# Kernel optimization log

Hardware: AMD Instinct MI355X
Metric: run time of the kernel (lower is better)

## Reference

```python
import jax, jax.numpy as jnp
import numpy as np

D_MODEL = 1024
NUM_HEADS = 16
D_K = D_MODEL // NUM_HEADS
B, S = 2, 2048


def setup_inputs() -> dict:
    key = jax.random.key(0)
    ks = jax.random.split(key, 13)
    s = 1.0 / np.sqrt(D_MODEL)
    inp = {
        "query": jax.random.normal(ks[0], (B, S, D_MODEL), jnp.float32),
        "key_": jax.random.normal(ks[1], (B, S, D_MODEL), jnp.float32),
        "value": jax.random.normal(ks[2], (B, S, D_MODEL), jnp.float32),
        "mask": jax.random.randint(ks[3], (B, 1, 1, S), 0, 2, jnp.int32),
        # torch nn.Linear convention: weight (out, in), y = x @ W.T + b
        "Wq": jax.random.uniform(ks[4], (D_MODEL, D_MODEL), jnp.float32, -s, s),
        "bq": jax.random.uniform(ks[5], (D_MODEL,), jnp.float32, -s, s),
        "Wk": jax.random.uniform(ks[6], (D_MODEL, D_MODEL), jnp.float32, -s, s),
        "bk": jax.random.uniform(ks[7], (D_MODEL,), jnp.float32, -s, s),
        "Wv": jax.random.uniform(ks[8], (D_MODEL, D_MODEL), jnp.float32, -s, s),
        "bv": jax.random.uniform(ks[9], (D_MODEL,), jnp.float32, -s, s),
        "Wo": jax.random.uniform(ks[10], (D_MODEL, D_MODEL), jnp.float32, -s, s),
        "bo": jax.random.uniform(ks[11], (D_MODEL,), jnp.float32, -s, s),
    }
    return inp


def _split_heads(x):
    b, s, _ = x.shape
    return x.reshape(b, s, NUM_HEADS, D_K).transpose(0, 2, 1, 3)  # (B,H,S,dk)


def reference(query, key_, value, mask, Wq, bq, Wk, bk, Wv, bv, Wo, bo):
    Q = _split_heads(query @ Wq.T + bq)
    K = _split_heads(key_ @ Wk.T + bk)
    V = _split_heads(value @ Wv.T + bv)
    scores = jnp.einsum("bhqd,bhkd->bhqk", Q, K) / np.sqrt(D_K).astype(np.float32)
    scores = jnp.where(mask == 0, -jnp.inf, scores)
    attn = jax.nn.softmax(scores, axis=-1)
    attn = jnp.nan_to_num(attn)  # fully-masked rows -> 0 (matches torch.nan_to_num)
    ctx = jnp.einsum("bhqk,bhkd->bhqd", attn, V)
    concat = ctx.transpose(0, 2, 1, 3).reshape(query.shape[0], -1, D_MODEL)
    out = concat @ Wo.T + bo  # dropout is identity in eval mode
    return out
```

## Files before the change

### kernel.cpp

```cpp
#include <hip/hip_runtime.h>
#include <math.h>

#define D_MODEL 1024
#define NUM_HEADS 16
#define DK 64
#define BATCH 2
#define SEQ 2048

using f32x4  = __attribute__((ext_vector_type(4))) float;
using f16x8  = __attribute__((ext_vector_type(8))) _Float16;

__device__ __forceinline__ void gl_lds16(const void* g, void* l) {
    __builtin_amdgcn_global_load_lds(
        (const __attribute__((address_space(1))) void*)g,
        (__attribute__((address_space(3))) void*)l, 16, 0, 0);
}

__global__ __launch_bounds__(256) void mask_scan_kernel(
    const int* __restrict__ mask, int* __restrict__ pos, int* __restrict__ nc)
{
    const int b = blockIdx.x;
    const int tid = threadIdx.x;
    __shared__ int sums[256];
    int v[8]; int cnt = 0;
    const int base = b * SEQ + tid * 8;
    #pragma unroll
    for (int e = 0; e < 8; ++e) { v[e] = (mask[base + e] != 0) ? 1 : 0; cnt += v[e]; }
    sums[tid] = cnt;
    __syncthreads();
    for (int off = 1; off < 256; off <<= 1) {
        int t = (tid >= off) ? sums[tid - off] : 0;
        __syncthreads();
        sums[tid] += t;
        __syncthreads();
    }
    int run = sums[tid] - cnt;
    #pragma unroll
    for (int e = 0; e < 8; ++e) { pos[base + e] = run; run += v[e]; }
    if (tid == 255) nc[b] = sums[255];
}

template <int COMPACT>
__global__ __launch_bounds__(256) void conv_f16_kernel(
    const float* s0, const float* s1, const float* s2, const float* s3,
    _Float16* d0, _Float16* d1, _Float16* d2, _Float16* d3,
    int rows, const int* __restrict__ mask, const int* __restrict__ pos)
{
    const int y = blockIdx.y;
    const float* src = (y == 0) ? s0 : (y == 1) ? s1 : (y == 2) ? s2 : s3;
    _Float16* dst = (y == 0) ? d0 : (y == 1) ? d1 : (y == 2) ? d2 : d3;
    const int id = blockIdx.x * 256 + threadIdx.x;
    if (id >= rows * 128) return;
    const int row = id >> 7;
    int drow = row;
    if (COMPACT && y != 0) {
        if (!mask[row]) return;
        drow = (row >> 11) * SEQ + pos[row];
    }
    const int s  = id & 127;
    const int g  = s >> 3, ss = s & 7;
    const int lb = ss ^ (drow & 7);

    const float* p = src + (size_t)row * 1024 + g * 64 + lb * 8;
    const float4 a = *(const float4*)p;
    const float4 bq = *(const float4*)(p + 4);
    f16x8 o;
    o[0] = (_Float16)a.x;  o[1] = (_Float16)a.y;
    o[2] = (_Float16)a.z;  o[3] = (_Float16)a.w;
    o[4] = (_Float16)bq.x; o[5] = (_Float16)bq.y;
    o[6] = (_Float16)bq.z; o[7] = (_Float16)bq.w;
    *(f16x8*)&dst[(size_t)drow * 1024 + s * 8] = o;
}

template <int MODE>
__global__ __launch_bounds__(256) void mfma_gemm_f16_kernel(
    const _Float16* __restrict__ A2, const _Float16* __restrict__ W2,
    const float* __restrict__ bias, float* __restrict__ Cf,
    _Float16* __restrict__ Ch, const int* __restrict__ ncArr)
{
    constexpr int KS = 1024;
    __shared__ f16x8 Asl[3][1024];
    __shared__ f16x8 Bsl[3][512];

    const int bm = blockIdx.x * 128, bn = blockIdx.y * 64;
    if (MODE == 2 || MODE == 3) {
        if ((bm & (SEQ - 1)) >= ncArr[bm >> 11]) return;
    }

    const int tid = threadIdx.x;
    const int wv = tid >> 6, ln = tid & 63;
    const int wm = wv >> 1, wn = wv & 1;
    const int x = ln & 15, y = ln >> 4;

    f32x4 acc[4][2] = {};

    const _Float16* Ab = A2 + (size_t)bm * KS;
    const _Float16* Bb = W2 + (size_t)bn * KS;
    const int srow = ln >> 3;
    const int scol = (ln & 7) * 8;

    auto stage = [&](int bufi, int kt) {
        #pragma unroll
        for (int c = 0; c < 4; ++c) {
            const int rowb = wv * 32 + c * 8;
            gl_lds16(Ab + (size_t)(rowb + srow) * KS + kt * 64 + scol,
                     &Asl[bufi][rowb << 3]);
        }
        #pragma unroll
        for (int c = 0; c < 2; ++c) {
            const int rowb = wv * 16 + c * 8;
            gl_lds16(Bb + (size_t)(rowb + srow) * KS + kt * 64 + scol,
                     &Bsl[bufi][rowb << 3]);
        }
    };

    stage(0, 0);
    stage(1, 1);

    int buf = 0, sbuf = 2;
    for (int kt = 0; kt < 16; ++kt) {
        if (kt < 15) asm volatile("s_waitcnt vmcnt(6)" ::: "memory");
        else         asm volatile("s_waitcnt vmcnt(0)" ::: "memory");
        __builtin_amdgcn_s_barrier();
        if (kt + 2 < 16) stage(sbuf, kt + 2);
        #pragma unroll
        for (int half = 0; half < 2; ++half) {
            f16x8 af[4], bfr[2];
            #pragma unroll
            for (int mf = 0; mf < 4; ++mf) {
                const int r = wm * 64 + mf * 16 + x;
                af[mf] = Asl[buf][(r << 3) | ((half * 4 + y) ^ (r & 7))];
            }
            #pragma unroll
            for (int nf = 0; nf < 2; ++nf) {
                const int r = wn * 32 + nf * 16 + x;
                bfr[nf] = Bsl[buf][(r << 3) | ((half * 4 + y) ^ (r & 7))];
            }
            #pragma unroll
            for (int mf = 0; mf < 4; ++mf)
                #pragma unroll
                for (int nf = 0; nf < 2; ++nf)
                    acc[mf][nf] = __builtin_amdgcn_mfma_f32_16x16x32_f16(
                        af[mf], bfr[nf], acc[mf][nf], 0, 0, 0);
        }
        buf  = (buf  == 2) ? 0 : buf  + 1;
        sbuf = (sbuf == 2) ? 0 : sbuf + 1;
    }

    #pragma unroll
    for (int nf = 0; nf < 2; ++nf) {
        const int n = bn + wn * 32 + nf * 16 + x;
        const float bv = bias[n];
        #pragma unroll
        for (int mf = 0; mf < 4; ++mf) {
            const int mbase = bm + wm * 64 + mf * 16 + y * 4;
            #pragma unroll
            for (int r = 0; r < 4; ++r) {
                const int m = mbase + r;
                const float v = acc[mf][nf][r] + bv;
                const int b = m >> 11, s = m & (SEQ - 1);
                const int hh = n >> 6, dd = n & 63;
                if (MODE == 0) {
                    Cf[(size_t)m * D_MODEL + n] = v;
                } else if (MODE == 1) {
                    const int blk = (dd >> 3) ^ (s & 7), i = dd & 7;
                    Ch[((size_t)((b * NUM_HEADS + hh) * SEQ + s)) * 64 +
                       blk * 8 + i] = (_Float16)(v * 0.125f);
                } else if (MODE == 2) {
                    if (s < ncArr[b]) {
                        const int blk = (dd >> 3) ^ (s & 7), i = dd & 7;
                        Ch[((size_t)((b * NUM_HEADS + hh) * SEQ + s)) * 64 +
                           blk * 8 + i] = (_Float16)v;
                    }
                } else {
                    if (s < ncArr[b]) {
                        const int tile = s >> 6, w = s & 63;
                        const int blk = (w >> 3) ^ (dd & 7), i = w & 7;
                        Ch[((size_t)((b * NUM_HEADS + hh) * DK + dd)) * SEQ +
                           tile * 64 + blk * 8 + i] = (_Float16)v;
                    }
                }
            }
        }
    }
}

__global__ __launch_bounds__(256, 3) void attn_mfma_kernel(
    const _Float16* __restrict__ Q2, const _Float16* __restrict__ K2,
    const _Float16* __restrict__ VT2, const int* __restrict__ ncArr,
    _Float16* __restrict__ ACT)
{
    __shared__ __align__(16) _Float16 SM[20480];

    const int tid = threadIdx.x;
    const int wave = tid >> 6, lane = tid & 63;
    const int lo4 = lane & 15, hi4 = lane >> 4;
    _Float16* Pw = SM + 16384 + wave * 1024;

    const int orig = blockIdx.x;
    const int swz = (orig & 7) * 128 + (orig >> 3);
    const int bh = swz >> 5, qblk = swz & 31;
    const int b = bh >> 4, h = bh & 15;

    const _Float16* Kb = K2 + (size_t)bh * SEQ * 64;
    const _Float16* Vb = VT2 + (size_t)bh * DK * SEQ;

    const int ncb = ncArr[b];
    const int ntiles = (ncb + 63) >> 6;

    const int qr = qblk * 64 + wave * 16 + lo4;
    const _Float16* Q2row = Q2 + (size_t)(bh * SEQ + qr) * 64;
    f16x8 qf[2];
    #pragma unroll
    for (int c = 0; c < 2; ++c)
        qf[c] = *(const f16x8*)&Q2row[(((c * 4 + hi4) ^ (qr & 7)) * 8)];

    auto stage_kv = [&](int base, int k0) {
        #pragma unroll
        for (int j = 0; j < 4; ++j) {
            const int g = j * 256 + wave * 64;
            const int gi = g + lane;
            const _Float16* src;
            if (gi < 512) {
                src = Kb + (size_t)(k0 + (gi >> 3)) * 64 + (gi & 7) * 8;
            } else {
                const int g2 = gi - 512;
                src = Vb + (size_t)(g2 >> 3) * SEQ + k0 + (g2 & 7) * 8;
            }
            gl_lds16(src, SM + base + (size_t)g * 8);
        }
    };

    f32x4 ctx[4] = {};
    float m = -INFINITY, l = 0.f;

    stage_kv(0, 0);
    for (int t = 0; t < ntiles; ++t) {
        if (t + 1 < ntiles) {
            stage_kv(((t + 1) & 1) * 8192, (t + 1) * 64);
            asm volatile("s_waitcnt vmcnt(4)" ::: "memory");
        } else {
            asm volatile("s_waitcnt vmcnt(0)" ::: "memory");
        }
        __builtin_amdgcn_s_barrier();

        const _Float16* Ks = SM + (t & 1) * 8192;
        const _Float16* VTs = Ks + 4096;
        const int k0 = t * 64;

        f32x4 sc[4];
        __builtin_amdgcn_s_setprio(1);
        #pragma unroll
        for (int kt = 0; kt < 4; ++kt) {
            f32x4 s = {0.f, 0.f, 0.f, 0.f};
            const int row = kt * 16 + lo4;
            const int rx = row & 7;
            #pragma unroll
            for (int c = 0; c < 2; ++c) {
                const f16x8 kf = *(f16x8*)&Ks[row * 64 + (((c * 4 + hi4) ^ rx) * 8)];
                s = __builtin_amdgcn_mfma_f32_16x16x32_f16(kf, qf[c], s, 0, 0, 0);
            }
            sc[kt] = s;
        }
        __builtin_amdgcn_s_setprio(0);

        float cmax = -1e30f;
        if (k0 + 64 <= ncb) {
            #pragma unroll
            for (int kt = 0; kt < 4; ++kt)
                #pragma unroll
                for (int r = 0; r < 4; ++r) cmax = fmaxf(cmax, sc[kt][r]);
        } else {
            #pragma unroll
            for (int kt = 0; kt < 4; ++kt)
                #pragma unroll
                for (int r = 0; r < 4; ++r) {
                    const int kidx = k0 + kt * 16 + hi4 * 4 + r;
                    const float sv = (kidx < ncb) ? sc[kt][r] : -1e30f;
                    sc[kt][r] = sv;
                    cmax = fmaxf(cmax, sv);
                }
        }
        cmax = fmaxf(cmax, __shfl_xor(cmax, 16));
        cmax = fmaxf(cmax, __shfl_xor(cmax, 32));

        const float mnew = fmaxf(m, cmax);
        const float e1 = __expf(m - mnew);
        m = mnew;

        float ps = 0.f;
        #pragma unroll
        for (int kt = 0; kt < 4; ++kt) {
            const float pv0 = __expf(sc[kt][0] - mnew);
            const float pv1 = __expf(sc[kt][1] - mnew);
            const float pv2 = __expf(sc[kt][2] - mnew);
            const float pv3 = __expf(sc[kt][3] - mnew);
            ps += (pv0 + pv1) + (pv2 + pv3);
            union { _Float16 hh[2]; unsigned u; } pk0, pk1;
            pk0.hh[0] = (_Float16)pv0; pk0.hh[1] = (_Float16)pv1;
            pk1.hh[0] = (_Float16)pv2; pk1.hh[1] = (_Float16)pv3;
            const int blk16 = (kt * 2 + (hi4 >> 1)) ^ (lo4 & 7);
            unsigned* dst = (unsigned*)&Pw[lo4 * 64 + blk16 * 8 + (hi4 & 1) * 4];
            dst[0] = pk0.u; dst[1] = pk1.u;
        }
        ps += __shfl_xor(ps, 16);
        ps += __shfl_xor(ps, 32);
        l = l * e1 + ps;

        #pragma unroll
        for (int dt = 0; dt < 4; ++dt)
            #pragma unroll
            for (int r = 0; r < 4; ++r) ctx[dt][r] *= e1;

        __builtin_amdgcn_s_setprio(1);
        #pragma unroll
        for (int c = 0; c < 2; ++c) {
            const f16x8 pf = *(f16x8*)&Pw[lo4 * 64 + (((c * 4 + hi4) ^ (lo4 & 7)) * 8)];
            #pragma unroll
            for (int dt = 0; dt < 4; ++dt) {
                const int row = dt * 16 + lo4;
                const f16x8 vf =
                    *(f16x8*)&VTs[row * 64 + (((c * 4 + hi4) ^ (row & 7)) * 8)];
                ctx[dt] = __builtin_amdgcn_mfma_f32_16x16x32_f16(vf, pf, ctx[dt], 0, 0, 0);
            }
        }
        __builtin_amdgcn_s_setprio(0);

        __builtin_amdgcn_s_barrier();
    }

    __syncthreads();
    const float inv = (l > 0.f) ? (1.f / l) : 0.f;
    float* OutL = (float*)SM;
    #pragma unroll
    for (int dt = 0; dt < 4; ++dt)
        #pragma unroll
        for (int r = 0; r < 4; ++r)
            OutL[(wave * 16 + lo4) * 68 + dt * 16 + hi4 * 4 + r] = ctx[dt][r] * inv;
    __syncthreads();
    {
        const int row = tid >> 2, cb = (tid & 3) * 16;
        const int mrow = b * SEQ + qblk * 64 + row;
        _Float16* arow = ACT + (size_t)mrow * 1024;
        #pragma unroll
        for (int u = 0; u < 2; ++u) {
            const int lb = (cb >> 3) + u;
            const int ss = lb ^ (mrow & 7);
            f16x8 hv;
            #pragma unroll
            for (int i = 0; i < 8; ++i)
                hv[i] = (_Float16)OutL[row * 68 + cb + u * 8 + i];
            *(f16x8*)&arow[h * 64 + ss * 8] = hv;
        }
    }
}

template <int SPLIT>
__global__ __launch_bounds__(256) void gemm_bias_kernel(
    const float* __restrict__ A, const float* __restrict__ W,
    const float* __restrict__ bias, float* __restrict__ C,
    int M, int N, int K)
{
    constexpr int TILE = 64, KT = 16;
    __shared__ float As[KT][TILE + 4];
    __shared__ float Ws[KT][TILE + 4];
    const int tid = threadIdx.x;
    const int tx = tid & 15, ty = tid >> 4;
    const int bm = blockIdx.x * TILE, bn = blockIdx.y * TILE;
    const int lrow = tid >> 2, lk4 = (tid & 3) << 2;
    float acc[4][4] = {{0.f}};
    for (int k0 = 0; k0 < K; k0 += KT) {
        const float4 a4 = *(const float4*)&A[(size_t)(bm + lrow) * K + k0 + lk4];
        const float4 w4 = *(const float4*)&W[(size_t)(bn + lrow) * K + k0 + lk4];
        __syncthreads();
        As[lk4 + 0][lrow] = a4.x; As[lk4 + 1][lrow] = a4.y;
        As[lk4 + 2][lrow] = a4.z; As[lk4 + 3][lrow] = a4.w;
        Ws[lk4 + 0][lrow] = w4.x; Ws[lk4 + 1][lrow] = w4.y;
        Ws[lk4 + 2][lrow] = w4.z; Ws[lk4 + 3][lrow] = w4.w;
        __syncthreads();
        #pragma unroll
        for (int kk = 0; kk < KT; ++kk) {
            const float4 av = *(const float4*)&As[kk][ty << 2];
            const float4 wv = *(const float4*)&Ws[kk][tx << 2];
            acc[0][0] += av.x * wv.x; acc[0][1] += av.x * wv.y; acc[0][2] += av.x * wv.z; acc[0][3] += av.x * wv.w;
            acc[1][0] += av.y * wv.x; acc[1][1] += av.y * wv.y; acc[1][2] += av.y * wv.z; acc[1][3] += av.y * wv.w;
            acc[2][0] += av.z * wv.x; acc[2][1] += av.z * wv.y; acc[2][2] += av.z * wv.z; acc[2][3] += av.z * wv.w;
            acc[3][0] += av.w * wv.x; acc[3][1] += av.w * wv.y; acc[3][2] += av.w * wv.z; acc[3][3] += av.w * wv.w;
        }
    }
    const float4 bb = *(const float4*)&bias[bn + (tx << 2)];
    #pragma unroll
    for (int i = 0; i < 4; ++i) {
        const int row = bm + (ty << 2) + i;
        float4 o;
        o.x = acc[i][0] + bb.x; o.y = acc[i][1] + bb.y;
        o.z = acc[i][2] + bb.z; o.w = acc[i][3] + bb.w;
        if (SPLIT) {
            const int b = row >> 11, s = row & (SEQ - 1), hh = bn >> 6;
            *(float4*)&C[((size_t)((b * NUM_HEADS + hh) * SEQ + s)) * DK + (tx << 2)] = o;
        } else {
            *(float4*)&C[(size_t)row * N + bn + (tx << 2)] = o;
        }
    }
}

__global__ __launch_bounds__(256, 2) void attn_fp32_kernel(
    const float* __restrict__ Q, const float* __restrict__ K,
    const float* __restrict__ V, const int* __restrict__ mask,
    float* __restrict__ OUT)
{
    const int qb = blockIdx.x, h = blockIdx.y, b = blockIdx.z;
    const int wave = threadIdx.x >> 6, lane = threadIdx.x & 63;
    const int tid = threadIdx.x;
    const int bh = b * NUM_HEADS + h;
    const float* Qb = Q + (size_t)bh * SEQ * DK;
    const float* Kb = K + (size_t)bh * SEQ * DK;
    const float* Vb = V + (size_t)bh * SEQ * DK;
    const int* mb = mask + b * SEQ;
    __shared__ float Ks[64][68];
    __shared__ float Vs[64][68];
    const int row = qb * 256 + wave * 64 + lane;
    float q[DK], ctx[DK];
    #pragma unroll
    for (int d4 = 0; d4 < 16; ++d4) {
        const float4 t = *(const float4*)&Qb[(size_t)row * DK + 4 * d4];
        q[4*d4] = t.x; q[4*d4+1] = t.y; q[4*d4+2] = t.z; q[4*d4+3] = t.w;
        ctx[4*d4] = 0.f; ctx[4*d4+1] = 0.f; ctx[4*d4+2] = 0.f; ctx[4*d4+3] = 0.f;
    }
    float m = -INFINITY, l = 0.f;
    for (int t = 0; t < SEQ / 64; ++t) {
        const int k0 = t * 64;
        const float* Kt = Kb + (size_t)k0 * DK;
        const float* Vt = Vb + (size_t)k0 * DK;
        __syncthreads();
        #pragma unroll
        for (int i = 0; i < 4; ++i) {
            const int f4 = i * 256 + tid;
            const int r = f4 >> 4, c = (f4 & 15) << 2;
            *(float4*)&Ks[r][c] = *(const float4*)&Kt[4 * f4];
            *(float4*)&Vs[r][c] = *(const float4*)&Vt[4 * f4];
        }
        __syncthreads();
        const unsigned long long mbits = __ballot(mb[k0 + lane] != 0);
        if (mbits == 0ULL) continue;
        for (int c0 = 0; c0 < 64; c0 += 16) {
            const unsigned bits = (unsigned)((mbits >> c0) & 0xFFFFULL);
            if (!bits) continue;
            float sc[16];
            #pragma unroll
            for (int j = 0; j < 16; ++j) {
                if (!((bits >> j) & 1u)) { sc[j] = -INFINITY; continue; }
                float a0 = 0.f, a1 = 0.f, a2 = 0.f, a3 = 0.f;
                #pragma unroll
                for (int d4 = 0; d4 < 16; ++d4) {
                    const float4 kv = *(const float4*)&Ks[c0 + j][4 * d4];
                    a0 += q[4*d4] * kv.x; a1 += q[4*d4+1] * kv.y;
                    a2 += q[4*d4+2] * kv.z; a3 += q[4*d4+3] * kv.w;
                }
                sc[j] = ((a0 + a1) + (a2 + a3)) * 0.125f;
            }
            float cmax = sc[0];
            #pragma unroll
            for (int j = 1; j < 16; ++j) cmax = fmaxf(cmax, sc[j]);
            if (cmax > m) {
                const float scale = __expf(m - cmax);
                l *= scale;
                #pragma unroll
                for (int d = 0; d < DK; ++d) ctx[d] *= scale;
                m = cmax;
            }
            #pragma unroll
            for (int j = 0; j < 16; ++j) {
                if (!((bits >> j) & 1u)) continue;
                const float p = __expf(sc[j] - m);
                l += p;
                #pragma unroll
                for (int d4 = 0; d4 < 16; ++d4) {
                    const float4 vv = *(const float4*)&Vs[c0 + j][4 * d4];
                    ctx[4*d4] += p * vv.x; ctx[4*d4+1] += p * vv.y;
                    ctx[4*d4+2] += p * vv.z; ctx[4*d4+3] += p * vv.w;
                }
            }
        }
    }
    const float inv = (l > 0.f) ? (1.f / l) : 0.f;
    float* dst = OUT + ((size_t)(b * SEQ + row)) * D_MODEL + h * DK;
    #pragma unroll
    for (int d4 = 0; d4 < 16; ++d4) {
        float4 o;
        o.x = ctx[4*d4] * inv; o.y = ctx[4*d4+1] * inv;
        o.z = ctx[4*d4+2] * inv; o.w = ctx[4*d4+3] * inv;
        *(float4*)&dst[4 * d4] = o;
    }
}

extern "C" void kernel_launch(void* const* d_in, const int* in_sizes, int n_in,
                              void* d_out, int out_size, void* d_ws, size_t ws_size,
                              hipStream_t stream)
{
    const float* query = (const float*)d_in[0];
    const float* key_  = (const float*)d_in[1];
    const float* value = (const float*)d_in[2];
    const int*   mask  = (const int*)d_in[3];
    const float* Wq = (const float*)d_in[4];
    const float* bq = (const float*)d_in[5];
    const float* Wk = (const float*)d_in[6];
    const float* bk = (const float*)d_in[7];
    const float* Wv = (const float*)d_in[8];
    const float* bv = (const float*)d_in[9];
    const float* Wo = (const float*)d_in[10];
    const float* bo = (const float*)d_in[11];
    float* out = (float*)d_out;

    const int M = BATCH * SEQ;
    const size_t ACT_B = (size_t)M * 1024 * 2;
    const size_t W_B   = (size_t)D_MODEL * 1024 * 2;
    const size_t K2_B  = (size_t)32 * SEQ * 64 * 2;
    const size_t VT2_B = (size_t)32 * DK * SEQ * 2;
    const size_t Q2_B  = K2_B;
    const size_t POS_B = (size_t)BATCH * SEQ * 4 + 256;

    char* base = (char*)d_ws;
    _Float16* actQh = (_Float16*)(base);
    _Float16* actKh = (_Float16*)(base + ACT_B);
    _Float16* actVh = (_Float16*)(base + 2 * ACT_B);
    _Float16* actO  = (_Float16*)(base + 3 * ACT_B);
    _Float16* w2qh  = (_Float16*)(base + 4 * ACT_B);
    _Float16* w2kh  = (_Float16*)((char*)w2qh + W_B);
    _Float16* w2vh  = (_Float16*)((char*)w2kh + W_B);
    _Float16* w2oh  = (_Float16*)((char*)w2vh + W_B);
    _Float16* k2    = (_Float16*)((char*)w2oh + W_B);
    _Float16* vt2   = (_Float16*)((char*)k2 + K2_B);
    _Float16* q2    = (_Float16*)((char*)vt2 + VT2_B);
    int* posArr = (int*)((char*)q2 + Q2_B);
    int* ncArr  = posArr + BATCH * SEQ;
    const size_t need = 4 * ACT_B + 4 * W_B + K2_B + VT2_B + Q2_B + POS_B;

    if (ws_size >= need) {
        mask_scan_kernel<<<BATCH, 256, 0, stream>>>(mask, posArr, ncArr);

        conv_f16_kernel<0><<<dim3(D_MODEL / 2, 4), 256, 0, stream>>>(
            Wq, Wk, Wv, Wo, w2qh, w2kh, w2vh, w2oh, D_MODEL, nullptr, nullptr);

        conv_f16_kernel<1><<<dim3(M / 2, 3), 256, 0, stream>>>(
            query, key_, value, nullptr, actQh, actKh, actVh, nullptr,
            M, mask, posArr);

        dim3 ggrid(M / 128, D_MODEL / 64);
        mfma_gemm_f16_kernel<2><<<ggrid, 256, 0, stream>>>(
            actKh, w2kh, bk, nullptr, k2, ncArr);
        mfma_gemm_f16_kernel<3><<<ggrid, 256, 0, stream>>>(
            actVh, w2vh, bv, nullptr, vt2, ncArr);
        mfma_gemm_f16_kernel<1><<<ggrid, 256, 0, stream>>>(
            actQh, w2qh, bq, nullptr, q2, ncArr);

        attn_mfma_kernel<<<1024, 256, 0, stream>>>(q2, k2, vt2, ncArr, actO);

        mfma_gemm_f16_kernel<0><<<ggrid, 256, 0, stream>>>(
            actO, w2oh, bo, out, nullptr, ncArr);
    } else {
        float* q_ws = (float*)(base);
        float* k_ws = (float*)(base + (size_t)M * D_MODEL * 4);
        float* v_ws = (float*)(base + 2 * (size_t)M * D_MODEL * 4);
        float* c_ws = (float*)(base + 3 * (size_t)M * D_MODEL * 4);
        dim3 ggrid(M / 64, D_MODEL / 64);
        gemm_bias_kernel<1><<<ggrid, 256, 0, stream>>>(query, Wq, bq, q_ws, M, D_MODEL, D_MODEL);
        gemm_bias_kernel<1><<<ggrid, 256, 0, stream>>>(key_,  Wk, bk, k_ws, M, D_MODEL, D_MODEL);
        gemm_bias_kernel<1><<<ggrid, 256, 0, stream>>>(value, Wv, bv, v_ws, M, D_MODEL, D_MODEL);
        dim3 agrid(SEQ / 256, NUM_HEADS, BATCH);
        attn_fp32_kernel<<<agrid, 256, 0, stream>>>(q_ws, k_ws, v_ws, mask, c_ws);
        gemm_bias_kernel<0><<<ggrid, 256, 0, stream>>>(c_ws, Wo, bo, out, M, D_MODEL, D_MODEL);
    }
}
```

Measured before the change: 134.0 us.

## Merge conversion and QKV GEMM launches, skip lazy rescale, raise attention occupancy

Combines the weight and activation fp16 conversion kernels into one 7-way launch and the three QKV projection GEMMs into a single 3D-grid launch, cutting launch count and tail idle time between kernels. The output projection gets its own specialized GEMM kernel. In attention, the running-max rescale of l and ctx is skipped when no lane's max grows, and the launch bound is raised to 4 blocks per CU. Runtime branching on z in the merged GEMM and possible register spills under the tighter occupancy bound are the risks.

```diff
diff --git a/kernel.cpp b/kernel.cpp
--- a/kernel.cpp
+++ b/kernel.cpp
@@ -40,20 +40,29 @@
     if (tid == 255) nc[b] = sums[255];
 }
 
-template <int COMPACT>
-__global__ __launch_bounds__(256) void conv_f16_kernel(
-    const float* s0, const float* s1, const float* s2, const float* s3,
-    _Float16* d0, _Float16* d1, _Float16* d2, _Float16* d3,
-    int rows, const int* __restrict__ mask, const int* __restrict__ pos)
+__global__ __launch_bounds__(256) void conv_all_kernel(
+    const float* Wq, const float* Wk, const float* Wv, const float* Wo,
+    const float* query, const float* key_, const float* value,
+    _Float16* w2q, _Float16* w2k, _Float16* w2v, _Float16* w2o,
+    _Float16* aq, _Float16* ak, _Float16* av,
+    const int* __restrict__ mask, const int* __restrict__ pos)
 {
     const int y = blockIdx.y;
-    const float* src = (y == 0) ? s0 : (y == 1) ? s1 : (y == 2) ? s2 : s3;
-    _Float16* dst = (y == 0) ? d0 : (y == 1) ? d1 : (y == 2) ? d2 : d3;
+    const float* src; _Float16* dst; int rows; bool compact = false;
+    switch (y) {
+        case 0: src = Wq;    dst = w2q; rows = 1024; break;
+        case 1: src = Wk;    dst = w2k; rows = 1024; break;
+        case 2: src = Wv;    dst = w2v; rows = 1024; break;
+        case 3: src = Wo;    dst = w2o; rows = 1024; break;
+        case 4: src = query; dst = aq;  rows = 4096; break;
+        case 5: src = key_;  dst = ak;  rows = 4096; compact = true; break;
+        default: src = value; dst = av; rows = 4096; compact = true; break;
+    }
     const int id = blockIdx.x * 256 + threadIdx.x;
     if (id >= rows * 128) return;
     const int row = id >> 7;
     int drow = row;
-    if (COMPACT && y != 0) {
+    if (compact) {
         if (!mask[row]) return;
         drow = (row >> 11) * SEQ + pos[row];
     }
@@ -72,18 +81,27 @@
     *(f16x8*)&dst[(size_t)drow * 1024 + s * 8] = o;
 }
 
-template <int MODE>
-__global__ __launch_bounds__(256) void mfma_gemm_f16_kernel(
-    const _Float16* __restrict__ A2, const _Float16* __restrict__ W2,
-    const float* __restrict__ bias, float* __restrict__ Cf,
-    _Float16* __restrict__ Ch, const int* __restrict__ ncArr)
+__global__ __launch_bounds__(256) void mfma_gemm_qkv_kernel(
+    const _Float16* __restrict__ aQ, const _Float16* __restrict__ aK,
+    const _Float16* __restrict__ aV,
+    const _Float16* __restrict__ wQ, const _Float16* __restrict__ wK,
+    const _Float16* __restrict__ wV,
+    const float* __restrict__ bQ, const float* __restrict__ bK,
+    const float* __restrict__ bV,
+    _Float16* __restrict__ q2, _Float16* __restrict__ k2,
+    _Float16* __restrict__ vt2, const int* __restrict__ ncArr)
 {
     constexpr int KS = 1024;
     __shared__ f16x8 Asl[3][1024];
     __shared__ f16x8 Bsl[3][512];
 
+    const int z = blockIdx.z;
+    const _Float16* A2 = (z == 0) ? aQ : (z == 1) ? aK : aV;
+    const _Float16* W2 = (z == 0) ? wQ : (z == 1) ? wK : wV;
+    const float* bias  = (z == 0) ? bQ : (z == 1) ? bK : bV;
+
     const int bm = blockIdx.x * 128, bn = blockIdx.y * 64;
-    if (MODE == 2 || MODE == 3) {
+    if (z != 0) {
         if ((bm & (SEQ - 1)) >= ncArr[bm >> 11]) return;
     }
 
@@ -160,24 +178,22 @@
                 const float v = acc[mf][nf][r] + bv;
                 const int b = m >> 11, s = m & (SEQ - 1);
                 const int hh = n >> 6, dd = n & 63;
-                if (MODE == 0) {
-                    Cf[(size_t)m * D_MODEL + n] = v;
-                } else if (MODE == 1) {
+                if (z == 0) {
                     const int blk = (dd >> 3) ^ (s & 7), i = dd & 7;
-                    Ch[((size_t)((b * NUM_HEADS + hh) * SEQ + s)) * 64 +
+                    q2[((size_t)((b * NUM_HEADS + hh) * SEQ + s)) * 64 +
                        blk * 8 + i] = (_Float16)(v * 0.125f);
-                } else if (MODE == 2) {
+                } else if (z == 1) {
                     if (s < ncArr[b]) {
                         const int blk = (dd >> 3) ^ (s & 7), i = dd & 7;
-                        Ch[((size_t)((b * NUM_HEADS + hh) * SEQ + s)) * 64 +
+                        k2[((size_t)((b * NUM_HEADS + hh) * SEQ + s)) * 64 +
                            blk * 8 + i] = (_Float16)v;
                     }
                 } else {
                     if (s < ncArr[b]) {
                         const int tile = s >> 6, w = s & 63;
                         const int blk = (w >> 3) ^ (dd & 7), i = w & 7;
-                        Ch[((size_t)((b * NUM_HEADS + hh) * DK + dd)) * SEQ +
-                           tile * 64 + blk * 8 + i] = (_Float16)v;
+                        vt2[((size_t)((b * NUM_HEADS + hh) * DK + dd)) * SEQ +
+                            tile * 64 + blk * 8 + i] = (_Float16)v;
                     }
                 }
             }
@@ -185,7 +201,92 @@
     }
 }
 
-__global__ __launch_bounds__(256, 3) void attn_mfma_kernel(
+__global__ __launch_bounds__(256) void mfma_gemm_o_kernel(
+    const _Float16* __restrict__ A2, const _Float16* __restrict__ W2,
+    const float* __restrict__ bias, float* __restrict__ Cf)
+{
+    constexpr int KS = 1024;
+    __shared__ f16x8 Asl[3][1024];
+    __shared__ f16x8 Bsl[3][512];
+
+    const int bm = blockIdx.x * 128, bn = blockIdx.y * 64;
+    const int tid = threadIdx.x;
+    const int wv = tid >> 6, ln = tid & 63;
+    const int wm = wv >> 1, wn = wv & 1;
+    const int x = ln & 15, y = ln >> 4;
+
+    f32x4 acc[4][2] = {};
+
+    const _Float16* Ab = A2 + (size_t)bm * KS;
+    const _Float16* Bb = W2 + (size_t)bn * KS;
+    const int srow = ln >> 3;
+    const int scol = (ln & 7) * 8;
+
+    auto stage = [&](int bufi, int kt) {
+        #pragma unroll
+        for (int c = 0; c < 4; ++c) {
+            const int rowb = wv * 32 + c * 8;
+            gl_lds16(Ab + (size_t)(rowb + srow) * KS + kt * 64 + scol,
+                     &Asl[bufi][rowb << 3]);
+        }
+        #pragma unroll
+        for (int c = 0; c < 2; ++c) {
+            const int rowb = wv * 16 + c * 8;
+            gl_lds16(Bb + (size_t)(rowb + srow) * KS + kt * 64 + scol,
+                     &Bsl[bufi][rowb << 3]);
+        }
+    };
+
+    stage(0, 0);
+    stage(1, 1);
+
+    int buf = 0, sbuf = 2;
+    for (int kt = 0; kt < 16; ++kt) {
+        if (kt < 15) asm volatile("s_waitcnt vmcnt(6)" ::: "memory");
+        else         asm volatile("s_waitcnt vmcnt(0)" ::: "memory");
+        __builtin_amdgcn_s_barrier();
+        if (kt + 2 < 16) stage(sbuf, kt + 2);
+        #pragma unroll
+        for (int half = 0; half < 2; ++half) {
+            f16x8 af[4], bfr[2];
+            #pragma unroll
+            for (int mf = 0; mf < 4; ++mf) {
+                const int r = wm * 64 + mf * 16 + x;
+                af[mf] = Asl[buf][(r << 3) | ((half * 4 + y) ^ (r & 7))];
+            }
+            #pragma unroll
+            for (int nf = 0; nf < 2; ++nf) {
+                const int r = wn * 32 + nf * 16 + x;
+                bfr[nf] = Bsl[buf][(r << 3) | ((half * 4 + y) ^ (r & 7))];
+            }
+            #pragma unroll
+            for (int mf = 0; mf < 4; ++mf)
+                #pragma unroll
+                for (int nf = 0; nf < 2; ++nf)
+                    acc[mf][nf] = __builtin_amdgcn_mfma_f32_16x16x32_f16(
+                        af[mf], bfr[nf], acc[mf][nf], 0, 0, 0);
+        }
+        buf  = (buf  == 2) ? 0 : buf  + 1;
+        sbuf = (sbuf == 2) ? 0 : sbuf + 1;
+    }
+
+    #pragma unroll
+    for (int nf = 0; nf < 2; ++nf) {
+        const int n = bn + wn * 32 + nf * 16 + x;
+        const float bv = bias[n];
+        #pragma unroll
+        for (int mf = 0; mf < 4; ++mf) {
+            const int mbase = bm + wm * 64 + mf * 16 + y * 4;
+            #pragma unroll
+            for (int r = 0; r < 4; ++r) {
+                const int m = mbase + r;
+                Cf[(size_t)m * D_MODEL + n] = acc[mf][nf][r] + bv;
+            }
+        }
+    }
+}
+
+__global__ __launch_bounds__(256, 4) void attn_mfma_kernel(
     const _Float16* __restrict__ Q2, const _Float16* __restrict__ K2,
     const _Float16* __restrict__ VT2, const int* __restrict__ ncArr,
     _Float16* __restrict__ ACT)
@@ -284,8 +385,9 @@
         cmax = fmaxf(cmax, __shfl_xor(cmax, 16));
         cmax = fmaxf(cmax, __shfl_xor(cmax, 32));
 
-        const float mnew = fmaxf(m, cmax);
-        const float e1 = __expf(m - mnew);
+        const bool grow = __any(cmax > m);
+        const float mold = m;
+        const float mnew = grow ? fmaxf(m, cmax) : m;
         m = mnew;
 
         float ps = 0.f;
@@ -305,12 +407,17 @@
         }
         ps += __shfl_xor(ps, 16);
         ps += __shfl_xor(ps, 32);
-        l = l * e1 + ps;
-
-        #pragma unroll
-        for (int dt = 0; dt < 4; ++dt)
-            #pragma unroll
-            for (int r = 0; r < 4; ++r) ctx[dt][r] *= e1;
+
+        if (grow) {
+            const float e1 = __expf(mold - mnew);
+            l = l * e1 + ps;
+            #pragma unroll
+            for (int dt = 0; dt < 4; ++dt)
+                #pragma unroll
+                for (int r = 0; r < 4; ++r) ctx[dt][r] *= e1;
+        } else {
+            l += ps;
+        }
 
         __builtin_amdgcn_s_setprio(1);
         #pragma unroll
@@ -539,25 +646,18 @@
     if (ws_size >= need) {
         mask_scan_kernel<<<BATCH, 256, 0, stream>>>(mask, posArr, ncArr);
 
-        conv_f16_kernel<0><<<dim3(D_MODEL / 2, 4), 256, 0, stream>>>(
-            Wq, Wk, Wv, Wo, w2qh, w2kh, w2vh, w2oh, D_MODEL, nullptr, nullptr);
-
-        conv_f16_kernel<1><<<dim3(M / 2, 3), 256, 0, stream>>>(
-            query, key_, value, nullptr, actQh, actKh, actVh, nullptr,
-            M, mask, posArr);
-
-        dim3 ggrid(M / 128, D_MODEL / 64);
-        mfma_gemm_f16_kernel<2><<<ggrid, 256, 0, stream>>>(
-            actKh, w2kh, bk, nullptr, k2, ncArr);
-        mfma_gemm_f16_kernel<3><<<ggrid, 256, 0, stream>>>(
-            actVh, w2vh, bv, nullptr, vt2, ncArr);
-        mfma_gemm_f16_kernel<1><<<ggrid, 256, 0, stream>>>(
-            actQh, w2qh, bq, nullptr, q2, ncArr);
+        conv_all_kernel<<<dim3(2048, 7), 256, 0, stream>>>(
+            Wq, Wk, Wv, Wo, query, key_, value,
+            w2qh, w2kh, w2vh, w2oh, actQh, actKh, actVh, mask, posArr);
+
+        mfma_gemm_qkv_kernel<<<dim3(M / 128, D_MODEL / 64, 3), 256, 0, stream>>>(
+            actQh, actKh, actVh, w2qh, w2kh, w2vh, bq, bk, bv,
+            q2, k2, vt2, ncArr);
 
         attn_mfma_kernel<<<1024, 256, 0, stream>>>(q2, k2, vt2, ncArr, actO);
 
-        mfma_gemm_f16_kernel<0><<<ggrid, 256, 0, stream>>>(
-            actO, w2oh, bo, out, nullptr, ncArr);
+        mfma_gemm_o_kernel<<<dim3(M / 128, D_MODEL / 64), 256, 0, stream>>>(
+            actO, w2oh, bo, out);
     } else {
         float* q_ws = (float*)(base);
         float* k_ws = (float*)(base + (size_t)M * D_MODEL * 4);
```

Result: no change. 133.3 us (-0.5%).

## Merge conversion launches, skip softmax rescale when max unchanged, raise attention occupancy

Applied to the files above, without the earlier changes.

The two fp32-to-fp16 conversion launches become one 7-slice grid, which saves a kernel launch but leaves many blocks in the weight slices doing nothing. In attention, the online-softmax rescale of ctx and l is skipped when no lane's running max grows, using a wave-wide vote. The attention kernel's launch-bounds hint rises from 3 to 4 blocks per SM to push for occupancy, at the risk of register spills.

```diff
diff --git a/kernel.cpp b/kernel.cpp
--- a/kernel.cpp
+++ b/kernel.cpp
@@ -40,20 +40,29 @@
     if (tid == 255) nc[b] = sums[255];
 }
 
-template <int COMPACT>
-__global__ __launch_bounds__(256) void conv_f16_kernel(
-    const float* s0, const float* s1, const float* s2, const float* s3,
-    _Float16* d0, _Float16* d1, _Float16* d2, _Float16* d3,
-    int rows, const int* __restrict__ mask, const int* __restrict__ pos)
+__global__ __launch_bounds__(256) void conv_all_kernel(
+    const float* Wq, const float* Wk, const float* Wv, const float* Wo,
+    const float* query, const float* key_, const float* value,
+    _Float16* w2q, _Float16* w2k, _Float16* w2v, _Float16* w2o,
+    _Float16* aq, _Float16* ak, _Float16* av,
+    const int* __restrict__ mask, const int* __restrict__ pos)
 {
     const int y = blockIdx.y;
-    const float* src = (y == 0) ? s0 : (y == 1) ? s1 : (y == 2) ? s2 : s3;
-    _Float16* dst = (y == 0) ? d0 : (y == 1) ? d1 : (y == 2) ? d2 : d3;
+    const float* src; _Float16* dst; int rows; bool compact = false;
+    switch (y) {
+        case 0: src = Wq;    dst = w2q; rows = 1024; break;
+        case 1: src = Wk;    dst = w2k; rows = 1024; break;
+        case 2: src = Wv;    dst = w2v; rows = 1024; break;
+        case 3: src = Wo;    dst = w2o; rows = 1024; break;
+        case 4: src = query; dst = aq;  rows = 4096; break;
+        case 5: src = key_;  dst = ak;  rows = 4096; compact = true; break;
+        default: src = value; dst = av; rows = 4096; compact = true; break;
+    }
     const int id = blockIdx.x * 256 + threadIdx.x;
     if (id >= rows * 128) return;
     const int row = id >> 7;
     int drow = row;
-    if (COMPACT && y != 0) {
+    if (compact) {
         if (!mask[row]) return;
         drow = (row >> 11) * SEQ + pos[row];
     }
@@ -185,7 +194,7 @@
     }
 }
 
-__global__ __launch_bounds__(256, 3) void attn_mfma_kernel(
+__global__ __launch_bounds__(256, 4) void attn_mfma_kernel(
     const _Float16* __restrict__ Q2, const _Float16* __restrict__ K2,
     const _Float16* __restrict__ VT2, const int* __restrict__ ncArr,
     _Float16* __restrict__ ACT)
@@ -284,8 +293,9 @@
         cmax = fmaxf(cmax, __shfl_xor(cmax, 16));
         cmax = fmaxf(cmax, __shfl_xor(cmax, 32));
 
-        const float mnew = fmaxf(m, cmax);
-        const float e1 = __expf(m - mnew);
+        const bool grow = __any(cmax > m);
+        const float mold = m;
+        const float mnew = grow ? fmaxf(m, cmax) : m;
         m = mnew;
 
         float ps = 0.f;
@@ -305,12 +315,17 @@
         }
         ps += __shfl_xor(ps, 16);
         ps += __shfl_xor(ps, 32);
-        l = l * e1 + ps;
-
-        #pragma unroll
-        for (int dt = 0; dt < 4; ++dt)
-            #pragma unroll
-            for (int r = 0; r < 4; ++r) ctx[dt][r] *= e1;
+
+        if (grow) {
+            const float e1 = __expf(mold - mnew);
+            l = l * e1 + ps;
+            #pragma unroll
+            for (int dt = 0; dt < 4; ++dt)
+                #pragma unroll
+                for (int r = 0; r < 4; ++r) ctx[dt][r] *= e1;
+        } else {
+            l += ps;
+        }
 
         __builtin_amdgcn_s_setprio(1);
         #pragma unroll
@@ -539,12 +554,9 @@
     if (ws_size >= need) {
         mask_scan_kernel<<<BATCH, 256, 0, stream>>>(mask, posArr, ncArr);
 
-        conv_f16_kernel<0><<<dim3(D_MODEL / 2, 4), 256, 0, stream>>>(
-            Wq, Wk, Wv, Wo, w2qh, w2kh, w2vh, w2oh, D_MODEL, nullptr, nullptr);
-
-        conv_f16_kernel<1><<<dim3(M / 2, 3), 256, 0, stream>>>(
-            query, key_, value, nullptr, actQh, actKh, actVh, nullptr,
-            M, mask, posArr);
+        conv_all_kernel<<<dim3(2048, 7), 256, 0, stream>>>(
+            Wq, Wk, Wv, Wo, query, key_, value,
+            w2qh, w2kh, w2vh, w2oh, actQh, actKh, actVh, mask, posArr);
 
         dim3 ggrid(M / 128, D_MODEL / 64);
         mfma_gemm_f16_kernel<2><<<ggrid, 256, 0, stream>>>(
```

Measured after the change: 130.7 us (median of 2 runs). 2.5% less time.
